# Kernel optimization log

Hardware: AMD Instinct MI355X
Metric: run time of the kernel (lower is better)

## Reference

```python
import jax, jax.numpy as jnp
import numpy as np

N, F, E, A, H = 50000, 64, 1600000, 8, 16
RECEPTIVE_FIELD = 7


def setup_inputs() -> dict:
    key = jax.random.key(0)
    ks = jax.random.split(key, 12)
    inp = {
        "x": jax.random.normal(ks[0], (N, F), dtype=jnp.float32),
        "edge_index": jax.random.randint(ks[1], (2, E), 0, N, dtype=jnp.int64),
        "w1": jax.random.normal(ks[2], (F, H), dtype=jnp.float32) * 0.1,
        "b1": jax.random.normal(ks[3], (H,), dtype=jnp.float32) * 0.1,
        "w2": jax.random.normal(ks[4], (H, H), dtype=jnp.float32) * 0.1,
        "b2": jax.random.normal(ks[5], (H,), dtype=jnp.float32) * 0.1,
        "w3": jax.random.normal(ks[6], (H, F), dtype=jnp.float32) * 0.1,
        "b3": jax.random.normal(ks[7], (F,), dtype=jnp.float32) * 0.1,
        "fc1_w": jax.random.normal(ks[8], ((1 + RECEPTIVE_FIELD) * F, F), dtype=jnp.float32) * 0.05,
        "fc1_b": jax.random.normal(ks[9], (F,), dtype=jnp.float32) * 0.05,
        "fc2_w": jax.random.normal(ks[10], (F, A), dtype=jnp.float32) * 0.1,
        "fc2_b": jax.random.normal(ks[11], (A,), dtype=jnp.float32) * 0.1,
    }
    return inp


def _mlp(x, w1, b1, w2, b2, w3, b3):
    h = jax.nn.relu(x @ w1 + b1)
    h = jax.nn.relu(h @ w2 + b2)
    return h @ w3 + b3


def _agg_mean(x, src, dst):
    # scatter-mean: mean of source-node features over incoming edges per target
    s = jax.ops.segment_sum(x[src], dst, num_segments=N)          # [N, F]
    cnt = jax.ops.segment_sum(jnp.ones((src.shape[0], 1), x.dtype), dst, num_segments=N)
    return s / jnp.maximum(cnt, 1.0)  # nodes with no in-edges -> 0 (torch mean aggr)


def reference(x, edge_index, w1, b1, w2, b2, w3, b3, fc1_w, fc1_b, fc2_w, fc2_b):
    src, dst = edge_index[0], edge_index[1]
    mlp = lambda t: _mlp(t, w1, b1, w2, b2, w3, b3)
    fields = [mlp(mlp(x))]
    for i in range(RECEPTIVE_FIELD):
        x_ = mlp(x)
        for _ in range(i + 1):
            x_ = _agg_mean(x_, src, dst)
        fields.append(mlp(x_))
    f = jnp.concatenate(fields, axis=1)          # [N, 8*F]
    h = f @ fc1_w + fc1_b                        # [N, F]
    logits = h @ fc2_w + fc2_b                   # [N, A]
    return jax.nn.softmax(logits, axis=-1)       # Categorical probs
```

## Files before the change

kernel.cpp:

```cpp
#include <hip/hip_runtime.h>


#define NB2MAX 400
#define NBLK   256
#define CAP2   32
#define CAPC   48
#define CAPB   6144
#define OVCAP  1024
#define LCAP   6144

__global__ __launch_bounds__(1024) void binfill_k(
    const int* __restrict__ src, const int* __restrict__ dst, int E, int n,
    int* __restrict__ gcur, int* __restrict__ ovbuf,
    int* __restrict__ bins, int* __restrict__ cnts,
    const float* __restrict__ w1, const float* __restrict__ w3,
    const float* __restrict__ b3, const float* __restrict__ fc1w,
    const float* __restrict__ fc1b, const float* __restrict__ fc2w,
    const float* __restrict__ fc2b,
    float* __restrict__ M, float* __restrict__ cvec,
    float* __restrict__ W31, float* __restrict__ c31) {
    __shared__ int lbuf[NB2MAX * CAP2];
    __shared__ int lcnt[NB2MAX];
    __shared__ int lflush[NB2MAX];
    int tid = threadIdx.x;
    int NB = (n + 127) >> 7;

    if ((int)blockIdx.x >= NBLK) {
        float* fl = (float*)lbuf;
        int s = (int)blockIdx.x - NBLK;
        if (s == 0) {
            if (tid < 256) {
                int i = tid >> 4, j = tid & 15;
                float a = 0.f;
                for (int g = 0; g < 64; g++) a += w3[i * 64 + g] * w1[g * 16 + j];
                W31[tid] = a;
            } else if (tid < 272) {
                int j = tid - 256;
                float a = 0.f;
                for (int g = 0; g < 64; g++) a += b3[g] * w1[g * 16 + j];
                c31[j] = a;
            } else if (tid >= 320 && tid < 384) {
                int h = tid - 320;
                float a = 0.f;
                for (int r = 0; r < 512; r++) a += b3[r & 63] * fc1w[r * 64 + h];
                fl[h] = a;
            }
            __syncthreads();
            if (tid < 8) {
                float a = fc2b[tid];
                for (int h = 0; h < 64; h++) a += (fc1b[h] + fl[h]) * fc2w[h * 8 + tid];
                cvec[tid] = a;
            }
        } else {
            int k = s - 1;
            {
                int i = tid >> 6, h = tid & 63;
                float a = 0.f;
                const float* f1 = fc1w + (size_t)(k * 64) * 64 + h;
                for (int g = 0; g < 64; g++) a += w3[i * 64 + g] * f1[g * 64];
                fl[i * 64 + h] = a;
            }
            __syncthreads();
            if (tid < 128) {
                int i = tid >> 3, j = tid & 7;
                float a = 0.f;
                for (int h = 0; h < 64; h++) a += fl[i * 64 + h] * fc2w[h * 8 + j];
                M[k * 128 + i * 8 + j] = a;
            }
        }
        return;
    }

    for (int b = tid; b < NB; b += 1024) { lcnt[b] = 0; lflush[b] = 0; }
    __syncthreads();
    int blk = blockIdx.x;
    int chunk = (E + NBLK - 1) / NBLK;
    int beg = blk * chunk;
    int end = beg + chunk; if (end > E) end = E;
    for (int t0 = beg; t0 < end; t0 += 1024) {
        int e = t0 + tid;
        if (e < end) {
            int d = dst[e], s = src[e];
            if ((unsigned)d < (unsigned)n && (unsigned)s < (unsigned)n) {
                int b = d >> 7;
                int pk = ((d & 127) << 16) | s;
                int pos = atomicAdd(&lcnt[b], 1);
                if (pos < CAP2) lbuf[b * CAP2 + pos] = pk;
                else {
                    int p = atomicAdd(&gcur[b], 1);
                    if (p < OVCAP) ovbuf[b * OVCAP + p] = pk;
                }
            }
        }
        __syncthreads();
        for (int b = tid; b < NB; b += 1024) {
            int cnt = lcnt[b]; if (cnt > CAP2) cnt = CAP2;
            int fl2 = lflush[b];
            size_t cell = ((size_t)b * NBLK + blk) * CAPC;
            int base = 0;
            while (cnt - base >= 16) {
                if (fl2 + 16 <= CAPC) {
                    int* dp = bins + cell + fl2;
                    #pragma unroll
                    for (int q = 0; q < 16; q++) dp[q] = lbuf[b * CAP2 + base + q];
                    fl2 += 16;
                } else {
                    int p = atomicAdd(&gcur[b], 16);
                    for (int q = 0; q < 16; q++)
                        if (p + q < OVCAP) ovbuf[b * OVCAP + p + q] = lbuf[b * CAP2 + base + q];
                }
                base += 16;
            }
            int rem = cnt - base;
            if (base > 0)
                for (int q = 0; q < rem; q++) lbuf[b * CAP2 + q] = lbuf[b * CAP2 + base + q];
            lcnt[b] = rem; lflush[b] = fl2;
        }
        __syncthreads();
    }
    for (int b = tid; b < NB; b += 1024) {
        int cnt = lcnt[b]; if (cnt > CAP2) cnt = CAP2;
        int fl2 = lflush[b];
        size_t cell = ((size_t)b * NBLK + blk) * CAPC;
        if (fl2 + cnt <= CAPC) {
            for (int q = 0; q < cnt; q++) bins[cell + fl2 + q] = lbuf[b * CAP2 + q];
            fl2 += cnt;
        } else {
            int p = atomicAdd(&gcur[b], cnt);
            for (int q = 0; q < cnt; q++)
                if (p + q < OVCAP) ovbuf[b * OVCAP + p + q] = lbuf[b * CAP2 + q];
        }
        cnts[(size_t)blk * NB + b] = fl2;
    }
}

__global__ __launch_bounds__(256) void csrproj_k(
    const int* __restrict__ bins, const int* __restrict__ cnts,
    const int* __restrict__ gcur, const int* __restrict__ ovbuf,
    int* __restrict__ csr, int2* __restrict__ be,
    const float* __restrict__ x, float* __restrict__ z0, float* __restrict__ logits,
    const float* __restrict__ w1, const float* __restrict__ b1,
    const float* __restrict__ w2, const float* __restrict__ b2,
    const float* __restrict__ W31, const float* __restrict__ c31,
    const float* __restrict__ M0, const float* __restrict__ cvec, int n) {
    int tid = threadIdx.x;
    int NB = (n + 127) >> 7;
    if ((int)blockIdx.x < NB) {
        __shared__ int hist[128], pref[128], cur[128];
        __shared__ int scnt[NBLK];
        __shared__ int lbuf[LCAP];
        __shared__ int sov;
        int b = blockIdx.x;
        if (tid < 128) { hist[tid] = 0; cur[tid] = 0; }
        scnt[tid] = cnts[(size_t)tid * NB + b];
        if (tid == 0) {
            int g = gcur[b];
            sov = g < 0 ? 0 : (g > OVCAP ? OVCAP : g);
        }
        __syncthreads();
        {
            int c = scnt[tid];
            size_t cell = ((size_t)b * NBLK + tid) * CAPC;
            for (int i = 0; i < c; i++) atomicAdd(&hist[bins[cell + i] >> 16], 1);
        }
        if (tid == 0)
            for (int i = 0; i < sov; i++) atomicAdd(&hist[ovbuf[b * OVCAP + i] >> 16], 1);
        __syncthreads();
        if (tid == 0) {
            int r = 0;
            for (int i = 0; i < 128; i++) { pref[i] = r; r += hist[i]; }
        }
        __syncthreads();
        if (tid < 128) {
            int d = (b << 7) + tid;
            if (d < n) {
                int bb = b * CAPB + pref[tid];
                be[d] = make_int2(bb, bb + hist[tid]);
            }
        }
        {
            int c = scnt[tid];
            size_t cell = ((size_t)b * NBLK + tid) * CAPC;
            for (int i = 0; i < c; i++) {
                int pk = bins[cell + i];
                int dl = pk >> 16;
                int pos = pref[dl] + atomicAdd(&cur[dl], 1);
                if (pos < LCAP) lbuf[pos] = pk & 0xffff;
            }
        }
        if (tid == 0) {
            for (int i = 0; i < sov; i++) {
                int pk = ovbuf[b * OVCAP + i];
                int dl = pk >> 16;
                int pos = pref[dl] + atomicAdd(&cur[dl], 1);
                if (pos < LCAP) lbuf[pos] = pk & 0xffff;
            }
        }
        __syncthreads();
        int nE = pref[127] + hist[127];
        if (nE > LCAP) nE = LCAP;
        for (int q = tid; q < nE; q += 256) csr[b * CAPB + q] = lbuf[q] << 2;
        return;
    }
    __shared__ float sw1[1024], sw2[256], sW[256], sM[128];
    __shared__ float sb1[16], sb2[16], sc[16], scv[8];
    for (int i = tid; i < 1024; i += 256) sw1[i] = w1[i];
    sw2[tid] = w2[tid & 255];
    sW[tid & 255] = W31[tid & 255];
    if (tid < 128) sM[tid] = M0[tid];
    if (tid < 16) { sb1[tid] = b1[tid]; sb2[tid] = b2[tid]; sc[tid] = c31[tid]; }
    if (tid < 8) scv[tid] = cvec[tid];
    __syncthreads();
    int nid = ((int)blockIdx.x - NB) * 256 + tid;
    if (nid >= n) return;
    float xr[64];
    const float4* xp = (const float4*)(x + (size_t)nid * 64);
    #pragma unroll
    for (int i = 0; i < 16; i++) {
        float4 v = xp[i];
        xr[4 * i] = v.x; xr[4 * i + 1] = v.y; xr[4 * i + 2] = v.z; xr[4 * i + 3] = v.w;
    }
    float t1[16];
    #pragma unroll
    for (int j = 0; j < 16; j++) {
        float a = sb1[j];
        #pragma unroll
        for (int f = 0; f < 64; f++) a += xr[f] * sw1[f * 16 + j];
        t1[j] = fmaxf(a, 0.f);
    }
    float t2[16];
    #pragma unroll
    for (int j = 0; j < 16; j++) {
        float a = sb2[j];
        #pragma unroll
        for (int i = 0; i < 16; i++) a += t1[i] * sw2[i * 16 + j];
        t2[j] = fmaxf(a, 0.f);
    }
    float z[16];
    #pragma unroll
    for (int j = 0; j < 16; j++) {
        float a = sc[j];
        #pragma unroll
        for (int i = 0; i < 16; i++) a += t2[i] * sW[i * 16 + j];
        z[j] = a;
    }
    float4* zo = (float4*)(z0 + (size_t)nid * 16);
    #pragma unroll
    for (int q = 0; q < 4; q++)
        zo[q] = make_float4(z[4 * q], z[4 * q + 1], z[4 * q + 2], z[4 * q + 3]);
    float h[16], f2[16];
    #pragma unroll
    for (int i = 0; i < 16; i++) h[i] = fmaxf(z[i] + sb1[i], 0.f);
    #pragma unroll
    for (int j = 0; j < 16; j++) {
        float a = sb2[j];
        #pragma unroll
        for (int i = 0; i < 16; i++) a += h[i] * sw2[i * 16 + j];
        f2[j] = fmaxf(a, 0.f);
    }
    float* lp = logits + (size_t)nid * 8;
    #pragma unroll
    for (int j = 0; j < 8; j++) {
        float l = scv[j];
        #pragma unroll
        for (int i = 0; i < 16; i++) l += f2[i] * sM[i * 8 + j];
        lp[j] = l;
    }
}

__global__ __launch_bounds__(256, 6) void hop_k(
    const float* __restrict__ zin, float* __restrict__ zout, float* __restrict__ logits,
    const int2* __restrict__ be, const int* __restrict__ csr,
    const float* __restrict__ w2, const float* __restrict__ b1,
    const float* __restrict__ b2, const float* __restrict__ M, int n, int FB) {
    __shared__ float sw2[256], sM[128], sb1[16], sb2[16];
    int tid = threadIdx.x;
    if ((int)blockIdx.x < FB) {
        sw2[tid] = w2[tid];
        if (tid < 128) sM[tid] = M[tid];
        if (tid < 16) { sb1[tid] = b1[tid]; sb2[tid] = b2[tid]; }
        __syncthreads();
        int nid = blockIdx.x * 256 + tid;
        if (nid >= n) return;
        float h[16];
        const float4* zp = (const float4*)(zin + (size_t)nid * 16);
        #pragma unroll
        for (int q = 0; q < 4; q++) {
            float4 v = zp[q];
            h[4 * q] = v.x; h[4 * q + 1] = v.y; h[4 * q + 2] = v.z; h[4 * q + 3] = v.w;
        }
        #pragma unroll
        for (int i = 0; i < 16; i++) h[i] = fmaxf(h[i] + sb1[i], 0.f);
        float t2[16];
        #pragma unroll
        for (int j = 0; j < 16; j++) {
            float a = sb2[j];
            #pragma unroll
            for (int i = 0; i < 16; i++) a += h[i] * sw2[i * 16 + j];
            t2[j] = fmaxf(a, 0.f);
        }
        float* lp = logits + (size_t)nid * 8;
        #pragma unroll
        for (int j = 0; j < 8; j++) {
            float l = 0.f;
            #pragma unroll
            for (int i = 0; i < 16; i++) l += t2[i] * sM[i * 8 + j];
            lp[j] += l;
        }
        return;
    }
    int node = ((int)blockIdx.x - FB) * 4 + (tid >> 6);
    if (node >= n) return;
    int lane = tid & 63;
    int e = lane >> 2, c = lane & 3;
    int2 b2e = be[node];
    int beg = b2e.x, end = b2e.y;
    int deg = end - beg;
    const float4* z4 = (const float4*)zin;
    float ax = 0.f, ay = 0.f, az = 0.f, aw = 0.f;
    int p = beg + e;
    if (deg <= 32) {
        int i0 = (p      < end) ? csr[p]      : -4;
        int i1 = (p + 16 < end) ? csr[p + 16] : -4;
        float4 v0 = z4[(size_t)(i0 < 0 ? 0 : i0) + c];
        float4 v1 = z4[(size_t)(i1 < 0 ? 0 : i1) + c];
        float s0 = i0 >= 0 ? 1.f : 0.f, s1 = i1 >= 0 ? 1.f : 0.f;
        ax += v0.x * s0 + v1.x * s1;
        ay += v0.y * s0 + v1.y * s1;
        az += v0.z * s0 + v1.z * s1;
        aw += v0.w * s0 + v1.w * s1;
    } else if (deg <= 48) {
        int i0 = csr[p];
        int i1 = csr[p + 16];
        int i2 = (p + 32 < end) ? csr[p + 32] : -4;
        float4 v0 = z4[(size_t)i0 + c];
        float4 v1 = z4[(size_t)i1 + c];
        float4 v2 = z4[(size_t)(i2 < 0 ? 0 : i2) + c];
        float s2 = i2 >= 0 ? 1.f : 0.f;
        ax += v0.x + v1.x + v2.x * s2;
        ay += v0.y + v1.y + v2.y * s2;
        az += v0.z + v1.z + v2.z * s2;
        aw += v0.w + v1.w + v2.w * s2;
    } else {
        int i0 = csr[p];
        int i1 = csr[p + 16];
        int i2 = csr[p + 32];
        int i3 = (p + 48 < end) ? csr[p + 48] : -4;
        float4 v0 = z4[(size_t)i0 + c];
        float4 v1 = z4[(size_t)i1 + c];
        float4 v2 = z4[(size_t)i2 + c];
        float4 v3 = z4[(size_t)(i3 < 0 ? 0 : i3) + c];
        float s3 = i3 >= 0 ? 1.f : 0.f;
        ax += v0.x + v1.x + v2.x + v3.x * s3;
        ay += v0.y + v1.y + v2.y + v3.y * s3;
        az += v0.z + v1.z + v2.z + v3.z * s3;
        aw += v0.w + v1.w + v2.w + v3.w * s3;
        for (p += 64; p < end; p += 16) {
            float4 v = z4[(size_t)csr[p] + c];
            ax += v.x; ay += v.y; az += v.z; aw += v.w;
        }
    }
    #pragma unroll
    for (int off = 32; off >= 4; off >>= 1) {
        ax += __shfl_down(ax, off);
        ay += __shfl_down(ay, off);
        az += __shfl_down(az, off);
        aw += __shfl_down(aw, off);
    }
    if (lane < 4) {
        float inv = 1.f / (float)(deg > 0 ? deg : 1);
        ((float4*)(zout + (size_t)node * 16))[lane] =
            make_float4(ax * inv, ay * inv, az * inv, aw * inv);
    }
}

__global__ __launch_bounds__(256) void fieldsoft_k(
    const float* __restrict__ z, float* __restrict__ logits,
    const float* __restrict__ w2, const float* __restrict__ b1,
    const float* __restrict__ b2, const float* __restrict__ M, int n) {
    __shared__ float sw2[256], sM[128], sb1[16], sb2[16];
    int tid = threadIdx.x;
    sw2[tid] = w2[tid];
    if (tid < 128) sM[tid] = M[tid];
    if (tid < 16) { sb1[tid] = b1[tid]; sb2[tid] = b2[tid]; }
    __syncthreads();
    int nid = blockIdx.x * 256 + tid;
    if (nid >= n) return;
    float h[16];
    const float4* zp = (const float4*)(z + (size_t)nid * 16);
    #pragma unroll
    for (int q = 0; q < 4; q++) {
        float4 v = zp[q];
        h[4 * q] = v.x; h[4 * q + 1] = v.y; h[4 * q + 2] = v.z; h[4 * q + 3] = v.w;
    }
    #pragma unroll
    for (int i = 0; i < 16; i++) h[i] = fmaxf(h[i] + sb1[i], 0.f);
    float t2[16];
    #pragma unroll
    for (int j = 0; j < 16; j++) {
        float a = sb2[j];
        #pragma unroll
        for (int i = 0; i < 16; i++) a += h[i] * sw2[i * 16 + j];
        t2[j] = fmaxf(a, 0.f);
    }
    float4* lp4 = (float4*)(logits + (size_t)nid * 8);
    float4 l0 = lp4[0], l1 = lp4[1];
    float v[8] = {l0.x, l0.y, l0.z, l0.w, l1.x, l1.y, l1.z, l1.w};
    #pragma unroll
    for (int j = 0; j < 8; j++) {
        float l = 0.f;
        #pragma unroll
        for (int i = 0; i < 16; i++) l += t2[i] * sM[i * 8 + j];
        v[j] += l;
    }
    float m = v[0];
    #pragma unroll
    for (int j = 1; j < 8; j++) m = fmaxf(m, v[j]);
    float s = 0.f;
    #pragma unroll
    for (int j = 0; j < 8; j++) { v[j] = expf(v[j] - m); s += v[j]; }
    float inv = 1.f / s;
    lp4[0] = make_float4(v[0] * inv, v[1] * inv, v[2] * inv, v[3] * inv);
    lp4[1] = make_float4(v[4] * inv, v[5] * inv, v[6] * inv, v[7] * inv);
}

extern "C" void kernel_launch(void* const* d_in, const int* in_sizes, int n_in,
                              void* d_out, int out_size, void* d_ws, size_t ws_size,
                              hipStream_t stream) {
    const float* x    = (const float*)d_in[0];
    const int*   ei   = (const int*)d_in[1];
    const float* w1   = (const float*)d_in[2];
    const float* b1   = (const float*)d_in[3];
    const float* w2   = (const float*)d_in[4];
    const float* b2   = (const float*)d_in[5];
    const float* w3   = (const float*)d_in[6];
    const float* b3   = (const float*)d_in[7];
    const float* fc1w = (const float*)d_in[8];
    const float* fc1b = (const float*)d_in[9];
    const float* fc2w = (const float*)d_in[10];
    const float* fc2b = (const float*)d_in[11];
    float* out = (float*)d_out;

    int n = in_sizes[0] / 64;
    int E = in_sizes[1] / 2;
    int NB = (n + 127) >> 7;
    const int* src = ei;
    const int* dst = ei + E;

    char* ws = (char*)d_ws;
    auto carve = [&](size_t bytes) {
        char* p = ws;
        ws += (bytes + 255) & ~((size_t)255);
        return p;
    };
    int*   gcur    = (int*)carve((size_t)NB * 4);
    int*   ovbuf   = (int*)carve((size_t)NB * OVCAP * 4);
    int*   binsbuf = (int*)carve((size_t)NB * NBLK * CAPC * 4);
    int*   cnts    = (int*)carve((size_t)NBLK * NB * 4);
    int*   csr     = (int*)carve((size_t)NB * CAPB * 4);
    int2*  be      = (int2*)carve((size_t)n * 8);
    float* buf0    = (float*)carve((size_t)n * 16 * 4);
    float* buf1    = (float*)carve((size_t)n * 16 * 4);
    float* M       = (float*)carve(1024 * 4);
    float* cvec    = (float*)carve(8 * 4);
    float* W31     = (float*)carve(256 * 4);
    float* c31     = (float*)carve(16 * 4);

    hipMemsetAsync(gcur, 0, (size_t)NB * 4, stream);
    binfill_k<<<NBLK + 9, 1024, 0, stream>>>(src, dst, E, n, gcur, ovbuf, binsbuf, cnts,
                                             w1, w3, b3, fc1w, fc1b, fc2w, fc2b,
                                             M, cvec, W31, c31);

    int FB = (n + 255) / 256;
    int AB = (n + 3) / 4;
    csrproj_k<<<NB + FB, 256, 0, stream>>>(binsbuf, cnts, gcur, ovbuf, csr, be,
                                           x, buf0, out, w1, b1, w2, b2, W31, c31,
                                           M, cvec, n);

    float* cur = buf0;
    float* nxt = buf1;
    hop_k<<<AB, 256, 0, stream>>>(cur, nxt, out, be, csr, w2, b1, b2, M, n, 0);
    { float* t = cur; cur = nxt; nxt = t; }
    for (int k = 1; k <= 6; k++) {
        hop_k<<<FB + AB, 256, 0, stream>>>(cur, nxt, out, be, csr,
                                           w2, b1, b2, M + k * 128, n, FB);
        float* t = cur; cur = nxt; nxt = t;
    }
    fieldsoft_k<<<FB, 256, 0, stream>>>(cur, out, w2, b1, b2, M + 7 * 128, n);
}
```

Before: 291.9 us.

## Use padded fixed-width neighbor lists with zero sentinel row for gather

Replaces the variable-length CSR used by the aggregation hops with a padded per-node array of 64 neighbor slots, where empty slots point to an extra zero-filled feature row. Each hop then does four unconditional gathers with no degree-based branching, and only falls back to the overflow CSR for nodes with more than 64 neighbors. The aim is to remove divergence and bounds checks in the hot gather loop. In exchange it writes a larger index buffer (n*64 ints) once and reads it every hop, including padding entries that all hit the sentinel row.

```diff
diff --git a/kernel.cpp b/kernel.cpp
--- a/kernel.cpp
+++ b/kernel.cpp
@@ -8,6 +8,7 @@
 #define CAPB   6144
 #define OVCAP  1024
 #define LCAP   6144
+#define CAPN   64
 
 __global__ __launch_bounds__(1024) void binfill_k(
     const int* __restrict__ src, const int* __restrict__ dst, int E, int n,
@@ -137,8 +138,10 @@
 __global__ __launch_bounds__(256) void csrproj_k(
     const int* __restrict__ bins, const int* __restrict__ cnts,
     const int* __restrict__ gcur, const int* __restrict__ ovbuf,
+    int* __restrict__ csrp, int* __restrict__ degs,
     int* __restrict__ csr, int2* __restrict__ be,
-    const float* __restrict__ x, float* __restrict__ z0, float* __restrict__ logits,
+    const float* __restrict__ x, float* __restrict__ z0, float* __restrict__ z1,
+    float* __restrict__ logits,
     const float* __restrict__ w1, const float* __restrict__ b1,
     const float* __restrict__ w2, const float* __restrict__ b2,
     const float* __restrict__ W31, const float* __restrict__ c31,
@@ -171,13 +174,6 @@
             for (int i = 0; i < 128; i++) { pref[i] = r; r += hist[i]; }
         }
         __syncthreads();
-        if (tid < 128) {
-            int d = (b << 7) + tid;
-            if (d < n) {
-                int bb = b * CAPB + pref[tid];
-                be[d] = make_int2(bb, bb + hist[tid]);
-            }
-        }
         {
             int c = scnt[tid];
             size_t cell = ((size_t)b * NBLK + tid) * CAPC;
@@ -197,9 +193,28 @@
             }
         }
         __syncthreads();
-        int nE = pref[127] + hist[127];
-        if (nE > LCAP) nE = LCAP;
-        for (int q = tid; q < nE; q += 256) csr[b * CAPB + q] = lbuf[q] << 2;
+        int SENT4 = n << 2;
+        for (int q = tid; q < 128 * CAPN; q += 256) {
+            int dl = q >> 6, j = q & 63;
+            int d = (b << 7) + dl;
+            if (d >= n) break;
+            int cnt = hist[dl];
+            int v = (j < cnt) ? (lbuf[pref[dl] + j] << 2) : SENT4;
+            csrp[(size_t)d * CAPN + j] = v;
+        }
+        if (tid < 128) {
+            int d = (b << 7) + tid;
+            if (d < n) {
+                int cnt = hist[tid];
+                degs[d] = cnt;
+                if (cnt > CAPN) {
+                    int s0 = b * CAPB + pref[tid];
+                    be[d] = make_int2(s0 + CAPN, s0 + cnt);
+                    for (int j = CAPN; j < cnt; j++)
+                        csr[s0 + j] = lbuf[pref[tid] + j] << 2;
+                }
+            }
+        }
         return;
     }
     __shared__ float sw1[1024], sw2[256], sW[256], sM[128];
@@ -211,6 +226,10 @@
     if (tid < 16) { sb1[tid] = b1[tid]; sb2[tid] = b2[tid]; sc[tid] = c31[tid]; }
     if (tid < 8) scv[tid] = cvec[tid];
     __syncthreads();
+    if ((int)blockIdx.x == NB && tid < 16) {
+        z0[(size_t)n * 16 + tid] = 0.f;
+        z1[(size_t)n * 16 + tid] = 0.f;
+    }
     int nid = ((int)blockIdx.x - NB) * 256 + tid;
     if (nid >= n) return;
     float xr[64];
@@ -270,6 +289,7 @@
 
 __global__ __launch_bounds__(256, 6) void hop_k(
     const float* __restrict__ zin, float* __restrict__ zout, float* __restrict__ logits,
+    const int* __restrict__ csrp, const int* __restrict__ degs,
     const int2* __restrict__ be, const int* __restrict__ csr,
     const float* __restrict__ w2, const float* __restrict__ b1,
     const float* __restrict__ b2, const float* __restrict__ M, int n, int FB) {
@@ -313,50 +333,25 @@
     if (node >= n) return;
     int lane = tid & 63;
     int e = lane >> 2, c = lane & 3;
-    int2 b2e = be[node];
-    int beg = b2e.x, end = b2e.y;
-    int deg = end - beg;
+    int degi = degs[node];
+    int p = (node << 6) + e;
+    int i0 = csrp[p];
+    int i1 = csrp[p + 16];
+    int i2 = csrp[p + 32];
+    int i3 = csrp[p + 48];
     const float4* z4 = (const float4*)zin;
-    float ax = 0.f, ay = 0.f, az = 0.f, aw = 0.f;
-    int p = beg + e;
-    if (deg <= 32) {
-        int i0 = (p      < end) ? csr[p]      : -4;
-        int i1 = (p + 16 < end) ? csr[p + 16] : -4;
-        float4 v0 = z4[(size_t)(i0 < 0 ? 0 : i0) + c];
-        float4 v1 = z4[(size_t)(i1 < 0 ? 0 : i1) + c];
-        float s0 = i0 >= 0 ? 1.f : 0.f, s1 = i1 >= 0 ? 1.f : 0.f;
-        ax += v0.x * s0 + v1.x * s1;
-        ay += v0.y * s0 + v1.y * s1;
-        az += v0.z * s0 + v1.z * s1;
-        aw += v0.w * s0 + v1.w * s1;
-    } else if (deg <= 48) {
-        int i0 = csr[p];
-        int i1 = csr[p + 16];
-        int i2 = (p + 32 < end) ? csr[p + 32] : -4;
-        float4 v0 = z4[(size_t)i0 + c];
-        float4 v1 = z4[(size_t)i1 + c];
-        float4 v2 = z4[(size_t)(i2 < 0 ? 0 : i2) + c];
-        float s2 = i2 >= 0 ? 1.f : 0.f;
-        ax += v0.x + v1.x + v2.x * s2;
-        ay += v0.y + v1.y + v2.y * s2;
-        az += v0.z + v1.z + v2.z * s2;
-        aw += v0.w + v1.w + v2.w * s2;
-    } else {
-        int i0 = csr[p];
-        int i1 = csr[p + 16];
-        int i2 = csr[p + 32];
-        int i3 = (p + 48 < end) ? csr[p + 48] : -4;
-        float4 v0 = z4[(size_t)i0 + c];
-        float4 v1 = z4[(size_t)i1 + c];
-        float4 v2 = z4[(size_t)i2 + c];
-        float4 v3 = z4[(size_t)(i3 < 0 ? 0 : i3) + c];
-        float s3 = i3 >= 0 ? 1.f : 0.f;
-        ax += v0.x + v1.x + v2.x + v3.x * s3;
-        ay += v0.y + v1.y + v2.y + v3.y * s3;
-        az += v0.z + v1.z + v2.z + v3.z * s3;
-        aw += v0.w + v1.w + v2.w + v3.w * s3;
-        for (p += 64; p < end; p += 16) {
-            float4 v = z4[(size_t)csr[p] + c];
+    float4 v0 = z4[(size_t)i0 + c];
+    float4 v1 = z4[(size_t)i1 + c];
+    float4 v2 = z4[(size_t)i2 + c];
+    float4 v3 = z4[(size_t)i3 + c];
+    float ax = (v0.x + v1.x) + (v2.x + v3.x);
+    float ay = (v0.y + v1.y) + (v2.y + v3.y);
+    float az = (v0.z + v1.z) + (v2.z + v3.z);
+    float aw = (v0.w + v1.w) + (v2.w + v3.w);
+    if (degi > CAPN) {
+        int2 r = be[node];
+        for (int q = r.x + e; q < r.y; q += 16) {
+            float4 v = z4[(size_t)csr[q] + c];
             ax += v.x; ay += v.y; az += v.z; aw += v.w;
         }
     }
@@ -368,7 +363,7 @@
         aw += __shfl_down(aw, off);
     }
     if (lane < 4) {
-        float inv = 1.f / (float)(deg > 0 ? deg : 1);
+        float inv = 1.f / (float)(degi > 0 ? degi : 1);
         ((float4*)(zout + (size_t)node * 16))[lane] =
             make_float4(ax * inv, ay * inv, az * inv, aw * inv);
     }
@@ -457,10 +452,12 @@
     int*   ovbuf   = (int*)carve((size_t)NB * OVCAP * 4);
     int*   binsbuf = (int*)carve((size_t)NB * NBLK * CAPC * 4);
     int*   cnts    = (int*)carve((size_t)NBLK * NB * 4);
+    int*   csrp    = (int*)carve((size_t)n * CAPN * 4);
+    int*   degs    = (int*)carve((size_t)n * 4);
     int*   csr     = (int*)carve((size_t)NB * CAPB * 4);
     int2*  be      = (int2*)carve((size_t)n * 8);
-    float* buf0    = (float*)carve((size_t)n * 16 * 4);
-    float* buf1    = (float*)carve((size_t)n * 16 * 4);
+    float* buf0    = (float*)carve((size_t)(n + 1) * 16 * 4);
+    float* buf1    = (float*)carve((size_t)(n + 1) * 16 * 4);
     float* M       = (float*)carve(1024 * 4);
     float* cvec    = (float*)carve(8 * 4);
     float* W31     = (float*)carve(256 * 4);
@@ -473,16 +470,18 @@
 
     int FB = (n + 255) / 256;
     int AB = (n + 3) / 4;
-    csrproj_k<<<NB + FB, 256, 0, stream>>>(binsbuf, cnts, gcur, ovbuf, csr, be,
-                                           x, buf0, out, w1, b1, w2, b2, W31, c31,
-                                           M, cvec, n);
+    csrproj_k<<<NB + FB, 256, 0, stream>>>(binsbuf, cnts, gcur, ovbuf,
+                                           csrp, degs, csr, be,
+                                           x, buf0, buf1, out, w1, b1, w2, b2,
+                                           W31, c31, M, cvec, n);
 
     float* cur = buf0;
     float* nxt = buf1;
-    hop_k<<<AB, 256, 0, stream>>>(cur, nxt, out, be, csr, w2, b1, b2, M, n, 0);
+    hop_k<<<AB, 256, 0, stream>>>(cur, nxt, out, csrp, degs, be, csr,
+                                  w2, b1, b2, M, n, 0);
     { float* t = cur; cur = nxt; nxt = t; }
     for (int k = 1; k <= 6; k++) {
-        hop_k<<<FB + AB, 256, 0, stream>>>(cur, nxt, out, be, csr,
+        hop_k<<<FB + AB, 256, 0, stream>>>(cur, nxt, out, csrp, degs, be, csr,
                                            w2, b1, b2, M + k * 128, n, FB);
         float* t = cur; cur = nxt; nxt = t;
     }
```

New measurement: 291.2 us. About the same (-0.3%).
